# Performance work log

Measured on AMD Instinct MI355X. Metric: run time of the kernel, lower is better.

The kernel has to match this reference:

```python
import jax, jax.numpy as jnp
import numpy as np

N_NODES = 100000
N_EDGES = 1600000
NFEAT = 128
NHID = 128
NCLASS = 40
BN_EPS = 1e-5


def _glorot(key, shape):
    fan_in, fan_out = shape[1], shape[0]
    lim = (6.0 / (fan_in + fan_out)) ** 0.5
    return jax.random.uniform(key, shape, jnp.float32, -lim, lim)


def setup_inputs() -> dict:
    key = jax.random.key(0)
    ks = jax.random.split(key, 16)
    x = jax.random.normal(ks[0], (N_NODES, NFEAT), jnp.float32)
    src = jax.random.randint(ks[1], (N_EDGES,), 0, N_NODES, jnp.int64)
    dst = jax.random.randint(ks[2], (N_EDGES,), 0, N_NODES, jnp.int64)
    edge_index = jnp.stack([src, dst])  # [2, E]
    return {
        "x": x,
        "edge_index": edge_index,
        # conv1: nfeat -> nhid (lin_l with bias on aggregated msgs, lin_r no bias on root)
        "W1l": _glorot(ks[3], (NHID, NFEAT)), "b1": jnp.zeros((NHID,), jnp.float32),
        "W1r": _glorot(ks[4], (NHID, NFEAT)),
        # convx[0]: nhid -> nhid
        "Wxl": _glorot(ks[5], (NHID, NHID)), "bx": jnp.zeros((NHID,), jnp.float32),
        "Wxr": _glorot(ks[6], (NHID, NHID)),
        # conv2: nhid -> nclass
        "W2l": _glorot(ks[7], (NCLASS, NHID)), "b2": jnp.zeros((NCLASS,), jnp.float32),
        "W2r": _glorot(ks[8], (NCLASS, NHID)),
        # batch_norm3 (nhid) and batch_norm2 (nclass)
        "g3": jnp.ones((NHID,), jnp.float32), "be3": jnp.zeros((NHID,), jnp.float32),
        "g2": jnp.ones((NCLASS,), jnp.float32), "be2": jnp.zeros((NCLASS,), jnp.float32),
    }


def _sage_conv(x, src, dst, Wl, b, Wr):
    # mean aggregation of source features at destination nodes
    msg = x[src]                                                  # [E, F] gather
    agg = jax.ops.segment_sum(msg, dst, num_segments=N_NODES)    # [N, F] scatter-add
    cnt = jax.ops.segment_sum(jnp.ones((msg.shape[0],), x.dtype), dst, num_segments=N_NODES)
    mean = agg / jnp.maximum(cnt, 1.0)[:, None]                   # empty neighborhoods -> 0
    return mean @ Wl.T + b + x @ Wr.T


def _batch_norm(x, gamma, beta):
    mu = jnp.mean(x, axis=0)
    var = jnp.mean(jnp.square(x - mu), axis=0)  # biased var (training-mode BN)
    return (x - mu) * jax.lax.rsqrt(var + BN_EPS) * gamma + beta


def reference(x, edge_index, W1l, b1, W1r, Wxl, bx, Wxr, W2l, b2, W2r, g3, be3, g2, be2):
    src, dst = edge_index[0], edge_index[1]
    h = _sage_conv(x, src, dst, W1l, b1, W1r)      # conv1
    h = jax.nn.relu(h)
    # convx loop (nlayer - 2 == 1); dropout p=0 is identity
    h = _sage_conv(h, src, dst, Wxl, bx, Wxr)
    h = _batch_norm(h, g3, be3)                    # batch_norm3 (BN=True)
    h = jax.nn.relu(h)
    h = _sage_conv(h, src, dst, W2l, b2, W2r)      # conv2
    h = _batch_norm(h, g2, be2)                    # batch_norm2
    return h
```

## Files before the change

kernel.cpp:

```cpp
#include <hip/hip_runtime.h>
#include <hip/hip_bf16.h>

#define NN 100000
#define NE 1600000
#define NF 128
#define NC 40
#define BN_EPS 1e-5f

#define NB 256
#define NBU ((NN + 511) >> 9)
#define PT_TILE 4096
#define PT_GRID ((NE + PT_TILE - 1) / PT_TILE)
#define SBANK 32
#define NTILES (NN / 16)
#define LIN_GRID 1250
#define LIN80_GRID 512

typedef __attribute__((ext_vector_type(8))) short short8;
typedef __attribute__((ext_vector_type(4))) float float4v;
typedef __attribute__((ext_vector_type(4))) int int4v;

__device__ __forceinline__ unsigned short f2b(float f) {
    __hip_bfloat16 h = __float2bfloat16(f);
    return *reinterpret_cast<unsigned short*>(&h);
}
__device__ __forceinline__ float b2f_hi(unsigned u) { return __uint_as_float(u & 0xffff0000u); }
__device__ __forceinline__ float b2f_lo(unsigned u) { return __uint_as_float(u << 16); }


__global__ __launch_bounds__(256) void bhist_kernel(const int* __restrict__ dst,
                                                    int* __restrict__ bhist) {
    __shared__ int lh[NB];
    int tid = threadIdx.x;
    lh[tid] = 0;
    __syncthreads();
    int base = blockIdx.x * PT_TILE;
    int cnt = min(PT_TILE, NE - base);
    const int4v* d4 = (const int4v*)(dst + base);
    int cnt4 = cnt >> 2;
    for (int i = tid; i < cnt4; i += 256) {
        int4v d = __builtin_nontemporal_load(d4 + i);
        atomicAdd(&lh[d[0] >> 9], 1);
        atomicAdd(&lh[d[1] >> 9], 1);
        atomicAdd(&lh[d[2] >> 9], 1);
        atomicAdd(&lh[d[3] >> 9], 1);
    }
    __syncthreads();
    if (lh[tid]) atomicAdd(&bhist[tid], lh[tid]);
}

__global__ __launch_bounds__(256) void bscan_kernel(const int* __restrict__ bhist,
                                                    int* __restrict__ bbase,
                                                    int* __restrict__ bcur) {
    __shared__ int lds[NB];
    int t = threadIdx.x;
    int v = bhist[t];
    lds[t] = v;
    __syncthreads();
    for (int off = 1; off < NB; off <<= 1) {
        int u = (t >= off) ? lds[t - off] : 0;
        __syncthreads();
        lds[t] += u;
        __syncthreads();
    }
    int ex = lds[t] - v;
    bbase[t] = ex;
    bcur[t] = ex;
}

__global__ __launch_bounds__(256) void part_kernel(const int* __restrict__ src,
                                                   const int* __restrict__ dst,
                                                   int* __restrict__ bcur,
                                                   int2* __restrict__ stage) {
    __shared__ int2 pairs[PT_TILE];
    __shared__ int lhist[NB];
    __shared__ int gbase[NB];
    int tid = threadIdx.x;
    int base = blockIdx.x * PT_TILE;
    int cnt = min(PT_TILE, NE - base);
    int cnt4 = cnt >> 2;

    lhist[tid] = 0;
    __syncthreads();

    const int4v* d4 = (const int4v*)(dst + base);
    const int4v* s4 = (const int4v*)(src + base);
    for (int i = tid; i < cnt4; i += 256) {
        int4v d = __builtin_nontemporal_load(d4 + i);
        int4v s = __builtin_nontemporal_load(s4 + i);
#pragma unroll
        for (int j = 0; j < 4; ++j) {
            pairs[j * cnt4 + i] = make_int2(d[j], s[j]);
            atomicAdd(&lhist[d[j] >> 9], 1);
        }
    }
    __syncthreads();

    int c = lhist[tid];
    gbase[tid] = (c > 0) ? atomicAdd(&bcur[tid], c) : 0;
    lhist[tid] = 0;
    __syncthreads();

    for (int k = tid; k < cnt; k += 256) {
        int2 p = pairs[k];
        int b = p.x >> 9;
        int pos = atomicAdd(&lhist[b], 1);
        stage[gbase[b] + pos] = p;
    }
}


__global__ __launch_bounds__(512) void bucket_build_kernel(const long long* __restrict__ stage,
                                                           const int* __restrict__ bbase,
                                                           const int* __restrict__ bcur,
                                                           int* __restrict__ row_ptr,
                                                           float* __restrict__ inv_cnt,
                                                           int* __restrict__ csr) {
    __shared__ int hist[512];
    __shared__ int sa[512], sb[512];
    __shared__ int cur[512];
    int tid = threadIdx.x;
    int b = blockIdx.x;
    int s = bbase[b], e = bcur[b];

    hist[tid] = 0;
    __syncthreads();

    for (int i = s + tid; i < e; i += 512) {
        long long p = __builtin_nontemporal_load(stage + i);
        int dl = ((int)(p & 0xffffffffLL)) & 511;
        atomicAdd(&hist[dl], 1);
    }
    __syncthreads();

    sa[tid] = hist[tid];
    __syncthreads();
    int* pin = sa;
    int* pout = sb;
    for (int off = 1; off < 512; off <<= 1) {
        pout[tid] = pin[tid] + ((tid >= off) ? pin[tid - off] : 0);
        __syncthreads();
        int* t = pin; pin = pout; pout = t;
    }

    int d = hist[tid];
    int ex = pin[tid] - d;
    cur[tid] = ex;
    int n = b * 512 + tid;
    if (n < NN) {
        row_ptr[n] = s + ex;
        inv_cnt[n] = 1.0f / (float)(d > 0 ? d : 1);
    }
    if (b == 0 && tid == 0) row_ptr[NN] = NE;
    __syncthreads();

    for (int i = s + tid; i < e; i += 512) {
        long long p = __builtin_nontemporal_load(stage + i);
        int dl = ((int)(p & 0xffffffffLL)) & 511;
        int sv = (int)(p >> 32);
        int pos = atomicAdd(&cur[dl], 1);
        csr[s + pos] = sv;
    }
}


__global__ __launch_bounds__(256) void f2b4_kernel(const float* __restrict__ in,
                                                   unsigned short* __restrict__ out, int n4) {
    int i = blockIdx.x * 256 + threadIdx.x;
    if (i < n4) {
        float4 v = ((const float4*)in)[i];
        ushort4 o;
        o.x = f2b(v.x); o.y = f2b(v.y); o.z = f2b(v.z); o.w = f2b(v.w);
        ((ushort4*)out)[i] = o;
    }
}


__global__ __launch_bounds__(64) void pack_w_kernel(const float* __restrict__ Wl,
                                                    const float* __restrict__ Wr,
                                                    unsigned short* __restrict__ Bp) {
    int nt = blockIdx.x & 7;
    int kk = blockIdx.x >> 3;
    int lane = threadIdx.x;
    int n = nt * 16 + (lane & 15);
    int kb = kk * 32 + (lane >> 4) * 8;
    size_t base = ((size_t)(kk * 8 + nt) * 64 + lane) * 8;
#pragma unroll
    for (int j = 0; j < 8; ++j) {
        int k = kb + j;
        float v = (k < NF) ? Wl[(size_t)n * NF + k] : Wr[(size_t)n * NF + (k - NF)];
        Bp[base + j] = f2b(v);
    }
}

__global__ __launch_bounds__(64) void pack_w80_kernel(const float* __restrict__ Wl,
                                                      const float* __restrict__ Wr,
                                                      unsigned short* __restrict__ Bp) {
    int nt = blockIdx.x % 5;
    int kk = blockIdx.x / 5;
    int lane = threadIdx.x;
    int n = nt * 16 + (lane & 15);
    int kb = kk * 32 + (lane >> 4) * 8;
    size_t base = ((size_t)(kk * 5 + nt) * 64 + lane) * 8;
#pragma unroll
    for (int j = 0; j < 8; ++j) {
        int k = kb + j;
        float v = (n < NC) ? Wl[(size_t)n * NF + k] : Wr[(size_t)(n - NC) * NF + k];
        Bp[base + j] = f2b(v);
    }
}


__global__ __launch_bounds__(256) void agg_mean_bf16(const unsigned short* __restrict__ X,
                                                     const int* __restrict__ csr,
                                                     const int* __restrict__ row_ptr,
                                                     const float* __restrict__ inv_cnt,
                                                     unsigned short* __restrict__ out) {
    int tid = threadIdx.x;
    int lane = tid & 63;
    int wave = tid >> 6;
    int qw = lane >> 4;
    int sl = lane & 15;
    int n = blockIdx.x * 16 + wave * 4 + qw;
    if (n >= NN) return;
    int s = row_ptr[n], e = row_ptr[n + 1];
    int foff = sl * 8;

    float a[8];
#pragma unroll
    for (int j = 0; j < 8; ++j) a[j] = 0.f;

    int i = s;
    for (; i + 4 <= e; i += 4) {
        int s0 = csr[i], s1 = csr[i + 1], s2 = csr[i + 2], s3 = csr[i + 3];
        uint4 u0 = *(const uint4*)(X + (size_t)s0 * NF + foff);
        uint4 u1 = *(const uint4*)(X + (size_t)s1 * NF + foff);
        uint4 u2 = *(const uint4*)(X + (size_t)s2 * NF + foff);
        uint4 u3 = *(const uint4*)(X + (size_t)s3 * NF + foff);
        a[0] += b2f_lo(u0.x) + b2f_lo(u1.x) + b2f_lo(u2.x) + b2f_lo(u3.x);
        a[1] += b2f_hi(u0.x) + b2f_hi(u1.x) + b2f_hi(u2.x) + b2f_hi(u3.x);
        a[2] += b2f_lo(u0.y) + b2f_lo(u1.y) + b2f_lo(u2.y) + b2f_lo(u3.y);
        a[3] += b2f_hi(u0.y) + b2f_hi(u1.y) + b2f_hi(u2.y) + b2f_hi(u3.y);
        a[4] += b2f_lo(u0.z) + b2f_lo(u1.z) + b2f_lo(u2.z) + b2f_lo(u3.z);
        a[5] += b2f_hi(u0.z) + b2f_hi(u1.z) + b2f_hi(u2.z) + b2f_hi(u3.z);
        a[6] += b2f_lo(u0.w) + b2f_lo(u1.w) + b2f_lo(u2.w) + b2f_lo(u3.w);
        a[7] += b2f_hi(u0.w) + b2f_hi(u1.w) + b2f_hi(u2.w) + b2f_hi(u3.w);
    }
    for (; i < e; ++i) {
        uint4 u = *(const uint4*)(X + (size_t)csr[i] * NF + foff);
        a[0] += b2f_lo(u.x); a[1] += b2f_hi(u.x);
        a[2] += b2f_lo(u.y); a[3] += b2f_hi(u.y);
        a[4] += b2f_lo(u.z); a[5] += b2f_hi(u.z);
        a[6] += b2f_lo(u.w); a[7] += b2f_hi(u.w);
    }

    float ic = inv_cnt[n];
    uint4 o;
    o.x = (unsigned)f2b(a[0] * ic) | ((unsigned)f2b(a[1] * ic) << 16);
    o.y = (unsigned)f2b(a[2] * ic) | ((unsigned)f2b(a[3] * ic) << 16);
    o.z = (unsigned)f2b(a[4] * ic) | ((unsigned)f2b(a[5] * ic) << 16);
    o.w = (unsigned)f2b(a[6] * ic) | ((unsigned)f2b(a[7] * ic) << 16);
    *(uint4*)(out + (size_t)n * NF + foff) = o;
}


template <bool RELU, bool STATS>
__device__ __forceinline__ void lin_body(const unsigned short* __restrict__ Ab,
                                         const unsigned short* __restrict__ Xb,
                                         const unsigned short* __restrict__ Bp,
                                         const float* __restrict__ bias,
                                         unsigned short* __restrict__ outb,
                                         float* __restrict__ sums,
                                         float* ls) {
    int tid = threadIdx.x;
    int wave = tid >> 6;
    int lane = tid & 63;
    int quad = lane >> 4;
    int sl = lane & 15;
    const short8* Bv = (const short8*)Bp;

    if (STATS) {
        ls[tid] = 0.f;
        __syncthreads();
    }

    short8 bfr[8][2];
#pragma unroll
    for (int kk = 0; kk < 8; ++kk)
#pragma unroll
        for (int j = 0; j < 2; ++j)
            bfr[kk][j] = Bv[(kk * 8 + 2 * wave + j) * 64 + lane];

    float4 bias4[2];
#pragma unroll
    for (int j = 0; j < 2; ++j)
        bias4[j] = *(const float4*)(bias + (2 * wave + j) * 16 + quad * 4);

    float sts[2][4], stq[2][4];
    if (STATS) {
#pragma unroll
        for (int j = 0; j < 2; ++j)
#pragma unroll
            for (int r = 0; r < 4; ++r) { sts[j][r] = 0.f; stq[j][r] = 0.f; }
    }

    for (int t = blockIdx.x; t < NTILES; t += LIN_GRID) {
        int rr = t * 16 + sl;
        const unsigned short* arow = Ab + (size_t)rr * NF;
        const unsigned short* xrow = Xb + (size_t)rr * NF;

        short8 xf[8];
#pragma unroll
        for (int kk = 0; kk < 8; ++kk) {
            int kb = (kk & 3) * 32 + quad * 8;
            const unsigned short* asrc = (kk < 4) ? arow : xrow;
            xf[kk] = *(const short8*)(asrc + kb);
        }

        float4v acc[2];
#pragma unroll
        for (int j = 0; j < 2; ++j) acc[j] = (float4v){0.f, 0.f, 0.f, 0.f};

#pragma unroll
        for (int kk = 0; kk < 8; ++kk)
#pragma unroll
            for (int j = 0; j < 2; ++j)
                acc[j] = __builtin_amdgcn_mfma_f32_16x16x32_bf16(bfr[kk][j], xf[kk], acc[j], 0, 0, 0);

#pragma unroll
        for (int j = 0; j < 2; ++j) {
            int c0 = (2 * wave + j) * 16 + quad * 4;
            float v0 = acc[j][0] + bias4[j].x;
            float v1 = acc[j][1] + bias4[j].y;
            float v2 = acc[j][2] + bias4[j].z;
            float v3 = acc[j][3] + bias4[j].w;
            if (RELU) {
                v0 = fmaxf(v0, 0.f); v1 = fmaxf(v1, 0.f);
                v2 = fmaxf(v2, 0.f); v3 = fmaxf(v3, 0.f);
            }
            if (STATS) {
                sts[j][0] += v0; stq[j][0] += v0 * v0;
                sts[j][1] += v1; stq[j][1] += v1 * v1;
                sts[j][2] += v2; stq[j][2] += v2 * v2;
                sts[j][3] += v3; stq[j][3] += v3 * v3;
            }
            ushort4 o;
            o.x = f2b(v0); o.y = f2b(v1); o.z = f2b(v2); o.w = f2b(v3);
            *(ushort4*)(outb + (size_t)rr * NF + c0) = o;
        }
    }

    if (STATS) {
#pragma unroll
        for (int j = 0; j < 2; ++j) {
            int c0 = (2 * wave + j) * 16 + quad * 4;
#pragma unroll
            for (int r = 0; r < 4; ++r) {
                atomicAdd(&ls[c0 + r], sts[j][r]);
                atomicAdd(&ls[128 + c0 + r], stq[j][r]);
            }
        }
        __syncthreads();
        atomicAdd(&sums[(blockIdx.x & (SBANK - 1)) * 256 + tid], ls[tid]);
    }
}

__global__ __launch_bounds__(256, 3) void lin_conv1_kernel(const unsigned short* __restrict__ Ab,
                                                           const unsigned short* __restrict__ Xb,
                                                           const unsigned short* __restrict__ Bp,
                                                           const float* __restrict__ bias,
                                                           unsigned short* __restrict__ outb) {
    lin_body<true, false>(Ab, Xb, Bp, bias, outb, nullptr, nullptr);
}

__global__ __launch_bounds__(256, 3) void lin_convx_kernel(const unsigned short* __restrict__ Ab,
                                                           const unsigned short* __restrict__ Xb,
                                                           const unsigned short* __restrict__ Bp,
                                                           const float* __restrict__ bias,
                                                           unsigned short* __restrict__ outb,
                                                           float* __restrict__ sums) {
    __shared__ float ls[256];
    lin_body<false, true>(Ab, Xb, Bp, bias, outb, sums, ls);
}


__global__ __launch_bounds__(128) void bn3_coef_kernel(const float* __restrict__ sums,
                                                       const float* __restrict__ g,
                                                       const float* __restrict__ be,
                                                       float* __restrict__ sc,
                                                       float* __restrict__ sh) {
    int c = threadIdx.x;
    float sv = 0.f, qv = 0.f;
    for (int b = 0; b < SBANK; ++b) {
        sv += sums[b * 256 + c];
        qv += sums[b * 256 + 128 + c];
    }
    float invN = 1.0f / (float)NN;
    float mu = sv * invN;
    float var = qv * invN - mu * mu;
    float s = rsqrtf(var + BN_EPS) * g[c];
    sc[c] = s;
    sh[c] = be[c] - mu * s;
}


__global__ __launch_bounds__(256, 2) void lin80_mfma_kernel(const unsigned short* __restrict__ Xb,
                                                            const unsigned short* __restrict__ Bp,
                                                            const float* __restrict__ b2,
                                                            const float* __restrict__ bnsc,
                                                            const float* __restrict__ bnsh,
                                                            unsigned short* __restrict__ t40,
                                                            float* __restrict__ z40) {
    int tid = threadIdx.x;
    int wave = tid >> 6;
    int lane = tid & 63;
    int quad = lane >> 4;
    int sl = lane & 15;
    const short8* Bv = (const short8*)Bp;

    short8 bfr[4][5];
#pragma unroll
    for (int kk = 0; kk < 4; ++kk)
#pragma unroll
        for (int nt = 0; nt < 5; ++nt)
            bfr[kk][nt] = Bv[(kk * 5 + nt) * 64 + lane];

    float4 sc0[4], sc1[4], sh0[4], sh1[4];
#pragma unroll
    for (int kk = 0; kk < 4; ++kk) {
        int kb = kk * 32 + quad * 8;
        sc0[kk] = *(const float4*)(bnsc + kb);
        sc1[kk] = *(const float4*)(bnsc + kb + 4);
        sh0[kk] = *(const float4*)(bnsh + kb);
        sh1[kk] = *(const float4*)(bnsh + kb + 4);
    }

    int gw = blockIdx.x * 4 + wave;
    for (int t = gw; t < NTILES; t += LIN80_GRID * 4) {
        int rr = t * 16 + sl;
        const unsigned short* xrow = Xb + (size_t)rr * NF;

        float4v acc[5];
#pragma unroll
        for (int nt = 0; nt < 5; ++nt) acc[nt] = (float4v){0.f, 0.f, 0.f, 0.f};

#pragma unroll
        for (int kk = 0; kk < 4; ++kk) {
            uint4 u = *(const uint4*)(xrow + kk * 32 + quad * 8);
            short8 xf;
            xf[0] = (short)f2b(fmaxf(b2f_lo(u.x) * sc0[kk].x + sh0[kk].x, 0.f));
            xf[1] = (short)f2b(fmaxf(b2f_hi(u.x) * sc0[kk].y + sh0[kk].y, 0.f));
            xf[2] = (short)f2b(fmaxf(b2f_lo(u.y) * sc0[kk].z + sh0[kk].z, 0.f));
            xf[3] = (short)f2b(fmaxf(b2f_hi(u.y) * sc0[kk].w + sh0[kk].w, 0.f));
            xf[4] = (short)f2b(fmaxf(b2f_lo(u.z) * sc1[kk].x + sh1[kk].x, 0.f));
            xf[5] = (short)f2b(fmaxf(b2f_hi(u.z) * sc1[kk].y + sh1[kk].y, 0.f));
            xf[6] = (short)f2b(fmaxf(b2f_lo(u.w) * sc1[kk].z + sh1[kk].z, 0.f));
            xf[7] = (short)f2b(fmaxf(b2f_hi(u.w) * sc1[kk].w + sh1[kk].w, 0.f));
#pragma unroll
            for (int nt = 0; nt < 5; ++nt)
                acc[nt] = __builtin_amdgcn_mfma_f32_16x16x32_bf16(bfr[kk][nt], xf, acc[nt], 0, 0, 0);
        }

#pragma unroll
        for (int nt = 0; nt < 5; ++nt) {
            int c0 = nt * 16 + quad * 4;
            if (c0 < NC) {
                ushort4 o;
                o.x = f2b(acc[nt][0]); o.y = f2b(acc[nt][1]);
                o.z = f2b(acc[nt][2]); o.w = f2b(acc[nt][3]);
                *(ushort4*)(t40 + (size_t)rr * NC + c0) = o;
            } else {
                float4 bz = *(const float4*)(b2 + c0 - NC);
                float4 o;
                o.x = acc[nt][0] + bz.x; o.y = acc[nt][1] + bz.y;
                o.z = acc[nt][2] + bz.z; o.w = acc[nt][3] + bz.w;
                *(float4*)(z40 + (size_t)rr * NC + (c0 - NC)) = o;
            }
        }
    }
}


__global__ __launch_bounds__(256) void agg40_add_bf16(const unsigned short* __restrict__ T,
                                                      const float* __restrict__ Z,
                                                      const int* __restrict__ csr,
                                                      const int* __restrict__ row_ptr,
                                                      const float* __restrict__ inv_cnt,
                                                      float* __restrict__ out) {
    int tid = threadIdx.x;
    int lane = tid & 63;
    int wave = tid >> 6;
    if (lane >= 60) return;
    int sub = lane / 20;
    int sl = lane % 20;
    int n = blockIdx.x * 12 + wave * 3 + sub;
    if (n >= NN) return;
    int s = row_ptr[n], e = row_ptr[n + 1];
    const unsigned short* Tf = T + sl * 2;
    float a0 = 0.f, a1 = 0.f;
    int i = s;
    for (; i + 4 <= e; i += 4) {
        int s0 = csr[i], s1 = csr[i + 1], s2 = csr[i + 2], s3 = csr[i + 3];
        unsigned u0 = *(const unsigned*)(Tf + (size_t)s0 * NC);
        unsigned u1 = *(const unsigned*)(Tf + (size_t)s1 * NC);
        unsigned u2 = *(const unsigned*)(Tf + (size_t)s2 * NC);
        unsigned u3 = *(const unsigned*)(Tf + (size_t)s3 * NC);
        a0 += b2f_lo(u0) + b2f_lo(u1) + b2f_lo(u2) + b2f_lo(u3);
        a1 += b2f_hi(u0) + b2f_hi(u1) + b2f_hi(u2) + b2f_hi(u3);
    }
    for (; i < e; ++i) {
        unsigned u = *(const unsigned*)(Tf + (size_t)csr[i] * NC);
        a0 += b2f_lo(u);
        a1 += b2f_hi(u);
    }
    float ic = inv_cnt[n];
    const float2 zv = *(const float2*)(Z + (size_t)n * NC + sl * 2);
    float2 o;
    o.x = a0 * ic + zv.x;
    o.y = a1 * ic + zv.y;
    *(float2*)(out + (size_t)n * NC + sl * 2) = o;
}

#define BN_GRID 640

template <int F>
__global__ __launch_bounds__(256) void bn_stats2_kernel(const float* __restrict__ X,
                                                        float* __restrict__ sums) {
    __shared__ float ls[2 * F];
    int tid = threadIdx.x;
    for (int i = tid; i < 2 * F; i += 256) ls[i] = 0.f;
    __syncthreads();

    const int total4 = NN * F / 4;
    const int stride = BN_GRID * 256;
    int i0 = blockIdx.x * 256 + tid;
    int c0 = (i0 * 4) % F;
    float s0 = 0.f, s1 = 0.f, s2 = 0.f, s3 = 0.f;
    float q0 = 0.f, q1 = 0.f, q2 = 0.f, q3 = 0.f;
    for (int i = i0; i < total4; i += stride) {
        float4 v = ((const float4*)X)[i];
        s0 += v.x; q0 += v.x * v.x;
        s1 += v.y; q1 += v.y * v.y;
        s2 += v.z; q2 += v.z * v.z;
        s3 += v.w; q3 += v.w * v.w;
    }
    atomicAdd(&ls[c0 + 0], s0); atomicAdd(&ls[F + c0 + 0], q0);
    atomicAdd(&ls[c0 + 1], s1); atomicAdd(&ls[F + c0 + 1], q1);
    atomicAdd(&ls[c0 + 2], s2); atomicAdd(&ls[F + c0 + 2], q2);
    atomicAdd(&ls[c0 + 3], s3); atomicAdd(&ls[F + c0 + 3], q3);
    __syncthreads();
    for (int i = tid; i < 2 * F; i += 256) atomicAdd(&sums[i], ls[i]);
}

template <bool RELU>
__global__ __launch_bounds__(256) void bn_apply_kernel(float* __restrict__ X,
                                                       const float* __restrict__ sums,
                                                       const float* __restrict__ g,
                                                       const float* __restrict__ be,
                                                       int F, float invN) {
    size_t idx = (size_t)blockIdx.x * blockDim.x + threadIdx.x;
    size_t total = (size_t)NN * F;
    if (idx >= total) return;
    int t = (int)(idx % F);
    float mu = sums[t] * invN;
    float var = sums[F + t] * invN - mu * mu;
    float scale = rsqrtf(var + BN_EPS) * g[t];
    float v = (X[idx] - mu) * scale + be[t];
    if (RELU) v = fmaxf(v, 0.f);
    X[idx] = v;
}


extern "C" void kernel_launch(void* const* d_in, const int* in_sizes, int n_in,
                              void* d_out, int out_size, void* d_ws, size_t ws_size,
                              hipStream_t stream) {
    const float* x   = (const float*)d_in[0];
    const int*   ei  = (const int*)d_in[1];
    const int*   srcv = ei;
    const int*   dstv = ei + NE;
    const float* W1l = (const float*)d_in[2];
    const float* b1  = (const float*)d_in[3];
    const float* W1r = (const float*)d_in[4];
    const float* Wxl = (const float*)d_in[5];
    const float* bx  = (const float*)d_in[6];
    const float* Wxr = (const float*)d_in[7];
    const float* W2l = (const float*)d_in[8];
    const float* b2  = (const float*)d_in[9];
    const float* W2r = (const float*)d_in[10];
    const float* g3  = (const float*)d_in[11];
    const float* be3 = (const float*)d_in[12];
    const float* g2  = (const float*)d_in[13];
    const float* be2 = (const float*)d_in[14];
    float* out = (float*)d_out;

    char* w = (char*)d_ws;
    unsigned short* xb   = (unsigned short*)w; w += (size_t)NN * NF * 2;
    unsigned short* h1b  = (unsigned short*)w; w += (size_t)NN * NF * 2;
    unsigned short* aggb = (unsigned short*)w; w += (size_t)NN * NF * 2;
    unsigned short* h2b  = (unsigned short*)w; w += (size_t)NN * NF * 2;
    int* csr     = (int*)w; w += (size_t)NE * 4;
    int* row_ptr = (int*)w; w += (size_t)(NN + 4) * 4;
    float* inv_cnt = (float*)w; w += (size_t)NN * 4;
    float* bnbuf3  = (float*)w; w += (size_t)SBANK * 256 * 4;
    float* bnbuf2  = (float*)w; w += 2 * NC * 4;
    float* bnsc    = (float*)w; w += NF * 4;
    float* bnsh    = (float*)w; w += NF * 4;
    unsigned short* Bp1 = (unsigned short*)w; w += (size_t)256 * NF * 2;
    unsigned short* Bpx = (unsigned short*)w; w += (size_t)256 * NF * 2;
    unsigned short* Bp2 = (unsigned short*)w; w += (size_t)128 * 80 * 2;
    int* bhist = (int*)w; w += NB * 4;
    int* bbase = (int*)w; w += NB * 4;
    int* bcurA = (int*)w; w += NB * 4;
    int2* stage = (int2*)h2b;
    unsigned short* t40 = xb;
    float* z40 = (float*)h1b;

    hipMemsetAsync(bhist, 0, NB * 4, stream);
    hipMemsetAsync(bnbuf3, 0, (size_t)SBANK * 256 * 4, stream);
    hipMemsetAsync(bnbuf2, 0, 2 * NC * 4, stream);

    bhist_kernel<<<PT_GRID, 256, 0, stream>>>(dstv, bhist);
    bscan_kernel<<<1, 256, 0, stream>>>(bhist, bbase, bcurA);
    part_kernel<<<PT_GRID, 256, 0, stream>>>(srcv, dstv, bcurA, stage);
    bucket_build_kernel<<<NBU, 512, 0, stream>>>((const long long*)stage, bbase, bcurA,
                                                 row_ptr, inv_cnt, csr);

    f2b4_kernel<<<(NN * NF / 4 + 255) / 256, 256, 0, stream>>>(x, xb, NN * NF / 4);
    pack_w_kernel<<<64, 64, 0, stream>>>(W1l, W1r, Bp1);
    pack_w_kernel<<<64, 64, 0, stream>>>(Wxl, Wxr, Bpx);
    pack_w80_kernel<<<20, 64, 0, stream>>>(W2l, W2r, Bp2);

    const int nblk_agg = (NN + 15) / 16;

    agg_mean_bf16<<<nblk_agg, 256, 0, stream>>>(xb, csr, row_ptr, inv_cnt, aggb);
    lin_conv1_kernel<<<LIN_GRID, 256, 0, stream>>>(aggb, xb, Bp1, b1, h1b);

    agg_mean_bf16<<<nblk_agg, 256, 0, stream>>>(h1b, csr, row_ptr, inv_cnt, aggb);
    lin_convx_kernel<<<LIN_GRID, 256, 0, stream>>>(aggb, h1b, Bpx, bx, h2b, bnbuf3);

    bn3_coef_kernel<<<1, 128, 0, stream>>>(bnbuf3, g3, be3, bnsc, bnsh);

    lin80_mfma_kernel<<<LIN80_GRID, 256, 0, stream>>>(h2b, Bp2, b2, bnsc, bnsh, t40, z40);
    agg40_add_bf16<<<(NN + 11) / 12, 256, 0, stream>>>(t40, z40, csr, row_ptr, inv_cnt, out);

    bn_stats2_kernel<NC><<<BN_GRID, 256, 0, stream>>>(out, bnbuf2);
    bn_apply_kernel<false><<<(NN * NC + 255) / 256, 256, 0, stream>>>(out, bnbuf2, g2, be2, NC, 1.0f / NN);
}
```

Before: 481.9 us.

## Fuse BN2 stats into agg40, restructure linear kernels with LDS weights and prefetch

The final batch-norm statistics are now accumulated inside the agg40 aggregation kernel through shared-memory atomics and 64 global banks. This removes a separate full pass over the output, and a small coefficient kernel then feeds a simpler per-element apply. The 128-wide linear kernels now use 512-thread blocks in which each wave handles one 16-column slice. Weights are staged in LDS, and each block processes a fixed run of 10 tiles with double-buffered row loads and scheduling barriers. The trade-offs are more LDS atomics in the aggregation kernel and higher LDS use per block in the linear kernels.

```diff
diff --git a/kernel.cpp b/kernel.cpp
--- a/kernel.cpp
+++ b/kernel.cpp
@@ -12,8 +12,10 @@
 #define PT_TILE 4096
 #define PT_GRID ((NE + PT_TILE - 1) / PT_TILE)
 #define SBANK 32
+#define NBANK2 64
 #define NTILES (NN / 16)
-#define LIN_GRID 1250
+#define LIN_BLKS 625
+#define TILES_PER_BLK 10
 #define LIN80_GRID 512
 
 typedef __attribute__((ext_vector_type(8))) short short8;
@@ -271,116 +273,107 @@
                                          const float* __restrict__ bias,
                                          unsigned short* __restrict__ outb,
                                          float* __restrict__ sums,
-                                         float* ls) {
+                                         short8* Bs, float* ls) {
     int tid = threadIdx.x;
-    int wave = tid >> 6;
+    int w = tid >> 6;
     int lane = tid & 63;
     int quad = lane >> 4;
     int sl = lane & 15;
+
     const short8* Bv = (const short8*)Bp;
-
-    if (STATS) {
-        ls[tid] = 0.f;
-        __syncthreads();
-    }
-
-    short8 bfr[8][2];
-#pragma unroll
-    for (int kk = 0; kk < 8; ++kk)
-#pragma unroll
-        for (int j = 0; j < 2; ++j)
-            bfr[kk][j] = Bv[(kk * 8 + 2 * wave + j) * 64 + lane];
-
-    float4 bias4[2];
-#pragma unroll
-    for (int j = 0; j < 2; ++j)
-        bias4[j] = *(const float4*)(bias + (2 * wave + j) * 16 + quad * 4);
-
-    float sts[2][4], stq[2][4];
-    if (STATS) {
-#pragma unroll
-        for (int j = 0; j < 2; ++j)
-#pragma unroll
-            for (int r = 0; r < 4; ++r) { sts[j][r] = 0.f; stq[j][r] = 0.f; }
-    }
-
-    for (int t = blockIdx.x; t < NTILES; t += LIN_GRID) {
+    for (int i = tid; i < 4096; i += 512) Bs[i] = Bv[i];
+    if (STATS && tid < 256) ls[tid] = 0.f;
+    __syncthreads();
+
+    float4 bias4 = *(const float4*)(bias + w * 16 + quad * 4);
+
+    float sv[4], qv[4];
+#pragma unroll
+    for (int r = 0; r < 4; ++r) { sv[r] = 0.f; qv[r] = 0.f; }
+
+    int tbase = blockIdx.x * TILES_PER_BLK;
+    short8 xa[8], xb_[8];
+
+    auto issue = [&](short8* buf, int t) {
         int rr = t * 16 + sl;
         const unsigned short* arow = Ab + (size_t)rr * NF;
         const unsigned short* xrow = Xb + (size_t)rr * NF;
-
-        short8 xf[8];
 #pragma unroll
         for (int kk = 0; kk < 8; ++kk) {
             int kb = (kk & 3) * 32 + quad * 8;
-            const unsigned short* asrc = (kk < 4) ? arow : xrow;
-            xf[kk] = *(const short8*)(asrc + kb);
-        }
-
-        float4v acc[2];
-#pragma unroll
-        for (int j = 0; j < 2; ++j) acc[j] = (float4v){0.f, 0.f, 0.f, 0.f};
-
-#pragma unroll
-        for (int kk = 0; kk < 8; ++kk)
-#pragma unroll
-            for (int j = 0; j < 2; ++j)
-                acc[j] = __builtin_amdgcn_mfma_f32_16x16x32_bf16(bfr[kk][j], xf[kk], acc[j], 0, 0, 0);
-
-#pragma unroll
-        for (int j = 0; j < 2; ++j) {
-            int c0 = (2 * wave + j) * 16 + quad * 4;
-            float v0 = acc[j][0] + bias4[j].x;
-            float v1 = acc[j][1] + bias4[j].y;
-            float v2 = acc[j][2] + bias4[j].z;
-            float v3 = acc[j][3] + bias4[j].w;
-            if (RELU) {
-                v0 = fmaxf(v0, 0.f); v1 = fmaxf(v1, 0.f);
-                v2 = fmaxf(v2, 0.f); v3 = fmaxf(v3, 0.f);
-            }
-            if (STATS) {
-                sts[j][0] += v0; stq[j][0] += v0 * v0;
-                sts[j][1] += v1; stq[j][1] += v1 * v1;
-                sts[j][2] += v2; stq[j][2] += v2 * v2;
-                sts[j][3] += v3; stq[j][3] += v3 * v3;
-            }
-            ushort4 o;
-            o.x = f2b(v0); o.y = f2b(v1); o.z = f2b(v2); o.w = f2b(v3);
-            *(ushort4*)(outb + (size_t)rr * NF + c0) = o;
-        }
+            buf[kk] = *(const short8*)(((kk < 4) ? arow : xrow) + kb);
+        }
+    };
+
+    auto compute = [&](short8* buf, int t) {
+        float4v acc = (float4v){0.f, 0.f, 0.f, 0.f};
+#pragma unroll
+        for (int kk = 0; kk < 8; ++kk) {
+            short8 bfr = Bs[(kk * 8 + w) * 64 + lane];
+            acc = __builtin_amdgcn_mfma_f32_16x16x32_bf16(bfr, buf[kk], acc, 0, 0, 0);
+        }
+        int rr = t * 16 + sl;
+        int c0 = w * 16 + quad * 4;
+        float v0 = acc[0] + bias4.x;
+        float v1 = acc[1] + bias4.y;
+        float v2 = acc[2] + bias4.z;
+        float v3 = acc[3] + bias4.w;
+        if (RELU) {
+            v0 = fmaxf(v0, 0.f); v1 = fmaxf(v1, 0.f);
+            v2 = fmaxf(v2, 0.f); v3 = fmaxf(v3, 0.f);
+        }
+        if (STATS) {
+            sv[0] += v0; qv[0] += v0 * v0;
+            sv[1] += v1; qv[1] += v1 * v1;
+            sv[2] += v2; qv[2] += v2 * v2;
+            sv[3] += v3; qv[3] += v3 * v3;
+        }
+        ushort4 o;
+        o.x = f2b(v0); o.y = f2b(v1); o.z = f2b(v2); o.w = f2b(v3);
+        *(ushort4*)(outb + (size_t)rr * NF + c0) = o;
+    };
+
+    issue(xa, tbase);
+#pragma unroll
+    for (int i = 0; i < TILES_PER_BLK; i += 2) {
+        issue(xb_, tbase + i + 1);
+        __builtin_amdgcn_sched_barrier(0);
+        compute(xa, tbase + i);
+        if (i + 2 < TILES_PER_BLK) issue(xa, tbase + i + 2);
+        __builtin_amdgcn_sched_barrier(0);
+        compute(xb_, tbase + i + 1);
     }
 
     if (STATS) {
-#pragma unroll
-        for (int j = 0; j < 2; ++j) {
-            int c0 = (2 * wave + j) * 16 + quad * 4;
-#pragma unroll
-            for (int r = 0; r < 4; ++r) {
-                atomicAdd(&ls[c0 + r], sts[j][r]);
-                atomicAdd(&ls[128 + c0 + r], stq[j][r]);
-            }
+        int c0 = w * 16 + quad * 4;
+#pragma unroll
+        for (int r = 0; r < 4; ++r) {
+            atomicAdd(&ls[c0 + r], sv[r]);
+            atomicAdd(&ls[128 + c0 + r], qv[r]);
         }
         __syncthreads();
-        atomicAdd(&sums[(blockIdx.x & (SBANK - 1)) * 256 + tid], ls[tid]);
-    }
-}
-
-__global__ __launch_bounds__(256, 3) void lin_conv1_kernel(const unsigned short* __restrict__ Ab,
+        if (tid < 256) atomicAdd(&sums[(blockIdx.x & (SBANK - 1)) * 256 + tid], ls[tid]);
+    }
+}
+
+__global__ __launch_bounds__(512, 4) void lin_conv1_kernel(const unsigned short* __restrict__ Ab,
                                                            const unsigned short* __restrict__ Xb,
                                                            const unsigned short* __restrict__ Bp,
                                                            const float* __restrict__ bias,
                                                            unsigned short* __restrict__ outb) {
-    lin_body<true, false>(Ab, Xb, Bp, bias, outb, nullptr, nullptr);
-}
-
-__global__ __launch_bounds__(256, 3) void lin_convx_kernel(const unsigned short* __restrict__ Ab,
+    __shared__ short8 Bs[4096];
+    lin_body<true, false>(Ab, Xb, Bp, bias, outb, nullptr, Bs, nullptr);
+}
+
+__global__ __launch_bounds__(512, 4) void lin_convx_kernel(const unsigned short* __restrict__ Ab,
                                                            const unsigned short* __restrict__ Xb,
                                                            const unsigned short* __restrict__ Bp,
                                                            const float* __restrict__ bias,
                                                            unsigned short* __restrict__ outb,
                                                            float* __restrict__ sums) {
+    __shared__ short8 Bs[4096];
     __shared__ float ls[256];
-    lin_body<false, true>(Ab, Xb, Bp, bias, outb, sums, ls);
+    lin_body<false, true>(Ab, Xb, Bp, bias, outb, sums, Bs, ls);
 }
 
 
@@ -486,88 +479,82 @@
                                                       const int* __restrict__ csr,
                                                       const int* __restrict__ row_ptr,
                                                       const float* __restrict__ inv_cnt,
-                                                      float* __restrict__ out) {
+                                                      float* __restrict__ out,
+                                                      float* __restrict__ sums2) {
+    __shared__ float ls[80];
     int tid = threadIdx.x;
+    if (tid < 80) ls[tid] = 0.f;
+    __syncthreads();
+
     int lane = tid & 63;
     int wave = tid >> 6;
-    if (lane >= 60) return;
     int sub = lane / 20;
     int sl = lane % 20;
     int n = blockIdx.x * 12 + wave * 3 + sub;
-    if (n >= NN) return;
-    int s = row_ptr[n], e = row_ptr[n + 1];
-    const unsigned short* Tf = T + sl * 2;
-    float a0 = 0.f, a1 = 0.f;
-    int i = s;
-    for (; i + 4 <= e; i += 4) {
-        int s0 = csr[i], s1 = csr[i + 1], s2 = csr[i + 2], s3 = csr[i + 3];
-        unsigned u0 = *(const unsigned*)(Tf + (size_t)s0 * NC);
-        unsigned u1 = *(const unsigned*)(Tf + (size_t)s1 * NC);
-        unsigned u2 = *(const unsigned*)(Tf + (size_t)s2 * NC);
-        unsigned u3 = *(const unsigned*)(Tf + (size_t)s3 * NC);
-        a0 += b2f_lo(u0) + b2f_lo(u1) + b2f_lo(u2) + b2f_lo(u3);
-        a1 += b2f_hi(u0) + b2f_hi(u1) + b2f_hi(u2) + b2f_hi(u3);
-    }
-    for (; i < e; ++i) {
-        unsigned u = *(const unsigned*)(Tf + (size_t)csr[i] * NC);
-        a0 += b2f_lo(u);
-        a1 += b2f_hi(u);
-    }
-    float ic = inv_cnt[n];
-    const float2 zv = *(const float2*)(Z + (size_t)n * NC + sl * 2);
-    float2 o;
-    o.x = a0 * ic + zv.x;
-    o.y = a1 * ic + zv.y;
-    *(float2*)(out + (size_t)n * NC + sl * 2) = o;
-}
-
-#define BN_GRID 640
-
-template <int F>
-__global__ __launch_bounds__(256) void bn_stats2_kernel(const float* __restrict__ X,
-                                                        float* __restrict__ sums) {
-    __shared__ float ls[2 * F];
-    int tid = threadIdx.x;
-    for (int i = tid; i < 2 * F; i += 256) ls[i] = 0.f;
-    __syncthreads();
-
-    const int total4 = NN * F / 4;
-    const int stride = BN_GRID * 256;
-    int i0 = blockIdx.x * 256 + tid;
-    int c0 = (i0 * 4) % F;
-    float s0 = 0.f, s1 = 0.f, s2 = 0.f, s3 = 0.f;
-    float q0 = 0.f, q1 = 0.f, q2 = 0.f, q3 = 0.f;
-    for (int i = i0; i < total4; i += stride) {
-        float4 v = ((const float4*)X)[i];
-        s0 += v.x; q0 += v.x * v.x;
-        s1 += v.y; q1 += v.y * v.y;
-        s2 += v.z; q2 += v.z * v.z;
-        s3 += v.w; q3 += v.w * v.w;
-    }
-    atomicAdd(&ls[c0 + 0], s0); atomicAdd(&ls[F + c0 + 0], q0);
-    atomicAdd(&ls[c0 + 1], s1); atomicAdd(&ls[F + c0 + 1], q1);
-    atomicAdd(&ls[c0 + 2], s2); atomicAdd(&ls[F + c0 + 2], q2);
-    atomicAdd(&ls[c0 + 3], s3); atomicAdd(&ls[F + c0 + 3], q3);
-    __syncthreads();
-    for (int i = tid; i < 2 * F; i += 256) atomicAdd(&sums[i], ls[i]);
-}
-
-template <bool RELU>
-__global__ __launch_bounds__(256) void bn_apply_kernel(float* __restrict__ X,
-                                                       const float* __restrict__ sums,
-                                                       const float* __restrict__ g,
-                                                       const float* __restrict__ be,
-                                                       int F, float invN) {
+    bool act = (lane < 60) && (n < NN);
+
+    if (act) {
+        int s = row_ptr[n], e = row_ptr[n + 1];
+        const unsigned short* Tf = T + sl * 2;
+        float a0 = 0.f, a1 = 0.f;
+        int i = s;
+        for (; i + 4 <= e; i += 4) {
+            int s0 = csr[i], s1 = csr[i + 1], s2 = csr[i + 2], s3 = csr[i + 3];
+            unsigned u0 = *(const unsigned*)(Tf + (size_t)s0 * NC);
+            unsigned u1 = *(const unsigned*)(Tf + (size_t)s1 * NC);
+            unsigned u2 = *(const unsigned*)(Tf + (size_t)s2 * NC);
+            unsigned u3 = *(const unsigned*)(Tf + (size_t)s3 * NC);
+            a0 += b2f_lo(u0) + b2f_lo(u1) + b2f_lo(u2) + b2f_lo(u3);
+            a1 += b2f_hi(u0) + b2f_hi(u1) + b2f_hi(u2) + b2f_hi(u3);
+        }
+        for (; i < e; ++i) {
+            unsigned u = *(const unsigned*)(Tf + (size_t)csr[i] * NC);
+            a0 += b2f_lo(u);
+            a1 += b2f_hi(u);
+        }
+        float ic = inv_cnt[n];
+        const float2 zv = *(const float2*)(Z + (size_t)n * NC + sl * 2);
+        float ox = a0 * ic + zv.x;
+        float oy = a1 * ic + zv.y;
+        float2 o; o.x = ox; o.y = oy;
+        *(float2*)(out + (size_t)n * NC + sl * 2) = o;
+        atomicAdd(&ls[2 * sl + 0], ox);
+        atomicAdd(&ls[2 * sl + 1], oy);
+        atomicAdd(&ls[NC + 2 * sl + 0], ox * ox);
+        atomicAdd(&ls[NC + 2 * sl + 1], oy * oy);
+    }
+    __syncthreads();
+    if (tid < 80) atomicAdd(&sums2[(blockIdx.x & (NBANK2 - 1)) * 80 + tid], ls[tid]);
+}
+
+
+__global__ __launch_bounds__(64) void bn2_coef_kernel(const float* __restrict__ sums2,
+                                                      const float* __restrict__ g,
+                                                      const float* __restrict__ be,
+                                                      float* __restrict__ sc,
+                                                      float* __restrict__ sh) {
+    int c = threadIdx.x;
+    if (c >= NC) return;
+    float s = 0.f, q = 0.f;
+    for (int b = 0; b < NBANK2; ++b) {
+        s += sums2[b * 80 + c];
+        q += sums2[b * 80 + NC + c];
+    }
+    float invN = 1.0f / (float)NN;
+    float mu = s * invN;
+    float var = q * invN - mu * mu;
+    float scv = rsqrtf(var + BN_EPS) * g[c];
+    sc[c] = scv;
+    sh[c] = be[c] - mu * scv;
+}
+
+__global__ __launch_bounds__(256) void bn2_apply_kernel(float* __restrict__ X,
+                                                        const float* __restrict__ sc,
+                                                        const float* __restrict__ sh) {
     size_t idx = (size_t)blockIdx.x * blockDim.x + threadIdx.x;
-    size_t total = (size_t)NN * F;
-    if (idx >= total) return;
-    int t = (int)(idx % F);
-    float mu = sums[t] * invN;
-    float var = sums[F + t] * invN - mu * mu;
-    float scale = rsqrtf(var + BN_EPS) * g[t];
-    float v = (X[idx] - mu) * scale + be[t];
-    if (RELU) v = fmaxf(v, 0.f);
-    X[idx] = v;
+    if (idx >= (size_t)NN * NC) return;
+    int c = (int)(idx % NC);
+    X[idx] = X[idx] * sc[c] + sh[c];
 }
 
 
@@ -602,9 +589,11 @@
     int* row_ptr = (int*)w; w += (size_t)(NN + 4) * 4;
     float* inv_cnt = (float*)w; w += (size_t)NN * 4;
     float* bnbuf3  = (float*)w; w += (size_t)SBANK * 256 * 4;
-    float* bnbuf2  = (float*)w; w += 2 * NC * 4;
+    float* sums2   = (float*)w; w += (size_t)NBANK2 * 80 * 4;
     float* bnsc    = (float*)w; w += NF * 4;
     float* bnsh    = (float*)w; w += NF * 4;
+    float* sc2     = (float*)w; w += 64 * 4;
+    float* sh2     = (float*)w; w += 64 * 4;
     unsigned short* Bp1 = (unsigned short*)w; w += (size_t)256 * NF * 2;
     unsigned short* Bpx = (unsigned short*)w; w += (size_t)256 * NF * 2;
     unsigned short* Bp2 = (unsigned short*)w; w += (size_t)128 * 80 * 2;
@@ -617,7 +606,7 @@
 
     hipMemsetAsync(bhist, 0, NB * 4, stream);
     hipMemsetAsync(bnbuf3, 0, (size_t)SBANK * 256 * 4, stream);
-    hipMemsetAsync(bnbuf2, 0, 2 * NC * 4, stream);
+    hipMemsetAsync(sums2, 0, (size_t)NBANK2 * 80 * 4, stream);
 
     bhist_kernel<<<PT_GRID, 256, 0, stream>>>(dstv, bhist);
     bscan_kernel<<<1, 256, 0, stream>>>(bhist, bbase, bcurA);
@@ -633,16 +622,16 @@
     const int nblk_agg = (NN + 15) / 16;
 
     agg_mean_bf16<<<nblk_agg, 256, 0, stream>>>(xb, csr, row_ptr, inv_cnt, aggb);
-    lin_conv1_kernel<<<LIN_GRID, 256, 0, stream>>>(aggb, xb, Bp1, b1, h1b);
+    lin_conv1_kernel<<<LIN_BLKS, 512, 0, stream>>>(aggb, xb, Bp1, b1, h1b);
 
     agg_mean_bf16<<<nblk_agg, 256, 0, stream>>>(h1b, csr, row_ptr, inv_cnt, aggb);
-    lin_convx_kernel<<<LIN_GRID, 256, 0, stream>>>(aggb, h1b, Bpx, bx, h2b, bnbuf3);
+    lin_convx_kernel<<<LIN_BLKS, 512, 0, stream>>>(aggb, h1b, Bpx, bx, h2b, bnbuf3);
 
     bn3_coef_kernel<<<1, 128, 0, stream>>>(bnbuf3, g3, be3, bnsc, bnsh);
 
     lin80_mfma_kernel<<<LIN80_GRID, 256, 0, stream>>>(h2b, Bp2, b2, bnsc, bnsh, t40, z40);
-    agg40_add_bf16<<<(NN + 11) / 12, 256, 0, stream>>>(t40, z40, csr, row_ptr, inv_cnt, out);
-
-    bn_stats2_kernel<NC><<<BN_GRID, 256, 0, stream>>>(out, bnbuf2);
-    bn_apply_kernel<false><<<(NN * NC + 255) / 256, 256, 0, stream>>>(out, bnbuf2, g2, be2, NC, 1.0f / NN);
-}
+    agg40_add_bf16<<<(NN + 11) / 12, 256, 0, stream>>>(t40, z40, csr, row_ptr, inv_cnt, out, sums2);
+
+    bn2_coef_kernel<<<1, 64, 0, stream>>>(sums2, g2, be2, sc2, sh2);
+    bn2_apply_kernel<<<(NN * NC + 255) / 256, 256, 0, stream>>>(out, sc2, sh2);
+}
```

Result: slower. 531.6 us (+10.3%).

## Split SAGE linear kernels by output half and double-buffer input tiles in LDS

Applied to the files above, without the earlier changes.

The two 128-wide SAGE linear kernels now launch twice as many blocks, each computing one half of the output columns. Weights are staged in shared memory, and the A/X row tiles are loaded coalesced into a swizzled, double-buffered LDS tile so the next tile's global load overlaps the current MFMA work. The BN stats bank count is doubled, and each half writes only its own channels. This trades register-resident weights for LDS reads plus per-tile barriers, and it re-reads the input rows once per column half.

```diff
diff --git a/kernel.cpp b/kernel.cpp
--- a/kernel.cpp
+++ b/kernel.cpp
@@ -11,9 +11,10 @@
 #define NBU ((NN + 511) >> 9)
 #define PT_TILE 4096
 #define PT_GRID ((NE + PT_TILE - 1) / PT_TILE)
-#define SBANK 32
+#define SBANK 64
 #define NTILES (NN / 16)
 #define LIN_GRID 1250
+#define LIN_TILES 5
 #define LIN80_GRID 512
 
 typedef __attribute__((ext_vector_type(8))) short short8;
@@ -271,97 +272,102 @@
                                          const float* __restrict__ bias,
                                          unsigned short* __restrict__ outb,
                                          float* __restrict__ sums,
-                                         float* ls) {
+                                         uint4* Bsv, uint4* Tls, float* ls) {
     int tid = threadIdx.x;
     int wave = tid >> 6;
     int lane = tid & 63;
     int quad = lane >> 4;
     int sl = lane & 15;
-    const short8* Bv = (const short8*)Bp;
+    int h = blockIdx.x & 1;
+    int b0 = blockIdx.x >> 1;
+    int nt = h * 4 + wave;
+
+    const uint4* Bg = (const uint4*)Bp;
+#pragma unroll
+    for (int j = 0; j < 8; ++j) {
+        int s = j * 256 + tid;
+        int l = s >> 6, ln = s & 63;
+        int gf = (l >> 2) * 8 + h * 4 + (l & 3);
+        Bsv[s] = Bg[gf * 64 + ln];
+    }
+    if (STATS) ls[tid] = 0.f;
+
+    int row0 = tid >> 4, cs = tid & 15;
+    int wslot = row0 * 16 + (cs ^ (row0 & 7));
+    {
+        int rr = b0 * 16 + row0;
+        uint4 ra = *(const uint4*)(Ab + (size_t)rr * NF + cs * 8);
+        uint4 rx = *(const uint4*)(Xb + (size_t)rr * NF + cs * 8);
+        Tls[wslot] = ra;
+        Tls[256 + wslot] = rx;
+    }
+    __syncthreads();
+
+    float4 bias4 = *(const float4*)(bias + nt * 16 + quad * 4);
+    float sv[4], qv[4];
+#pragma unroll
+    for (int r = 0; r < 4; ++r) { sv[r] = 0.f; qv[r] = 0.f; }
+
+#pragma unroll
+    for (int i = 0; i < LIN_TILES; ++i) {
+        const int cur = i & 1;
+        const int nxt = cur ^ 1;
+        int t = b0 + i * LIN_GRID;
+
+        uint4 ra, rx;
+        if (i + 1 < LIN_TILES) {
+            int rr1 = (b0 + (i + 1) * LIN_GRID) * 16 + row0;
+            ra = *(const uint4*)(Ab + (size_t)rr1 * NF + cs * 8);
+            rx = *(const uint4*)(Xb + (size_t)rr1 * NF + cs * 8);
+        }
+
+        float4v acc = (float4v){0.f, 0.f, 0.f, 0.f};
+#pragma unroll
+        for (int kk = 0; kk < 8; ++kk) {
+            int kcol = (kk & 3) * 4 + quad;
+            int xslot = cur * 512 + ((kk < 4) ? 0 : 256) + sl * 16 + (kcol ^ (sl & 7));
+            short8 xf = *(const short8*)(Tls + xslot);
+            short8 bf = *(const short8*)(Bsv + (kk * 4 + wave) * 64 + lane);
+            acc = __builtin_amdgcn_mfma_f32_16x16x32_bf16(bf, xf, acc, 0, 0, 0);
+        }
+
+        int rr = t * 16 + sl;
+        int c0 = nt * 16 + quad * 4;
+        float v0 = acc[0] + bias4.x;
+        float v1 = acc[1] + bias4.y;
+        float v2 = acc[2] + bias4.z;
+        float v3 = acc[3] + bias4.w;
+        if (RELU) {
+            v0 = fmaxf(v0, 0.f); v1 = fmaxf(v1, 0.f);
+            v2 = fmaxf(v2, 0.f); v3 = fmaxf(v3, 0.f);
+        }
+        if (STATS) {
+            sv[0] += v0; qv[0] += v0 * v0;
+            sv[1] += v1; qv[1] += v1 * v1;
+            sv[2] += v2; qv[2] += v2 * v2;
+            sv[3] += v3; qv[3] += v3 * v3;
+        }
+        ushort4 o;
+        o.x = f2b(v0); o.y = f2b(v1); o.z = f2b(v2); o.w = f2b(v3);
+        *(ushort4*)(outb + (size_t)rr * NF + c0) = o;
+
+        if (i + 1 < LIN_TILES) {
+            Tls[nxt * 512 + wslot] = ra;
+            Tls[nxt * 512 + 256 + wslot] = rx;
+        }
+        __syncthreads();
+    }
 
     if (STATS) {
-        ls[tid] = 0.f;
+        int c0 = nt * 16 + quad * 4;
+#pragma unroll
+        for (int r = 0; r < 4; ++r) {
+            atomicAdd(&ls[c0 + r], sv[r]);
+            atomicAdd(&ls[128 + c0 + r], qv[r]);
+        }
         __syncthreads();
-    }
-
-    short8 bfr[8][2];
-#pragma unroll
-    for (int kk = 0; kk < 8; ++kk)
-#pragma unroll
-        for (int j = 0; j < 2; ++j)
-            bfr[kk][j] = Bv[(kk * 8 + 2 * wave + j) * 64 + lane];
-
-    float4 bias4[2];
-#pragma unroll
-    for (int j = 0; j < 2; ++j)
-        bias4[j] = *(const float4*)(bias + (2 * wave + j) * 16 + quad * 4);
-
-    float sts[2][4], stq[2][4];
-    if (STATS) {
-#pragma unroll
-        for (int j = 0; j < 2; ++j)
-#pragma unroll
-            for (int r = 0; r < 4; ++r) { sts[j][r] = 0.f; stq[j][r] = 0.f; }
-    }
-
-    for (int t = blockIdx.x; t < NTILES; t += LIN_GRID) {
-        int rr = t * 16 + sl;
-        const unsigned short* arow = Ab + (size_t)rr * NF;
-        const unsigned short* xrow = Xb + (size_t)rr * NF;
-
-        short8 xf[8];
-#pragma unroll
-        for (int kk = 0; kk < 8; ++kk) {
-            int kb = (kk & 3) * 32 + quad * 8;
-            const unsigned short* asrc = (kk < 4) ? arow : xrow;
-            xf[kk] = *(const short8*)(asrc + kb);
-        }
-
-        float4v acc[2];
-#pragma unroll
-        for (int j = 0; j < 2; ++j) acc[j] = (float4v){0.f, 0.f, 0.f, 0.f};
-
-#pragma unroll
-        for (int kk = 0; kk < 8; ++kk)
-#pragma unroll
-            for (int j = 0; j < 2; ++j)
-                acc[j] = __builtin_amdgcn_mfma_f32_16x16x32_bf16(bfr[kk][j], xf[kk], acc[j], 0, 0, 0);
-
-#pragma unroll
-        for (int j = 0; j < 2; ++j) {
-            int c0 = (2 * wave + j) * 16 + quad * 4;
-            float v0 = acc[j][0] + bias4[j].x;
-            float v1 = acc[j][1] + bias4[j].y;
-            float v2 = acc[j][2] + bias4[j].z;
-            float v3 = acc[j][3] + bias4[j].w;
-            if (RELU) {
-                v0 = fmaxf(v0, 0.f); v1 = fmaxf(v1, 0.f);
-                v2 = fmaxf(v2, 0.f); v3 = fmaxf(v3, 0.f);
-            }
-            if (STATS) {
-                sts[j][0] += v0; stq[j][0] += v0 * v0;
-                sts[j][1] += v1; stq[j][1] += v1 * v1;
-                sts[j][2] += v2; stq[j][2] += v2 * v2;
-                sts[j][3] += v3; stq[j][3] += v3 * v3;
-            }
-            ushort4 o;
-            o.x = f2b(v0); o.y = f2b(v1); o.z = f2b(v2); o.w = f2b(v3);
-            *(ushort4*)(outb + (size_t)rr * NF + c0) = o;
-        }
-    }
-
-    if (STATS) {
-#pragma unroll
-        for (int j = 0; j < 2; ++j) {
-            int c0 = (2 * wave + j) * 16 + quad * 4;
-#pragma unroll
-            for (int r = 0; r < 4; ++r) {
-                atomicAdd(&ls[c0 + r], sts[j][r]);
-                atomicAdd(&ls[128 + c0 + r], stq[j][r]);
-            }
-        }
-        __syncthreads();
-        atomicAdd(&sums[(blockIdx.x & (SBANK - 1)) * 256 + tid], ls[tid]);
+        if (((tid & 127) >> 6) == h)
+            atomicAdd(&sums[(blockIdx.x & (SBANK - 1)) * 256 + tid], ls[tid]);
     }
 }
 
@@ -370,7 +376,9 @@
                                                            const unsigned short* __restrict__ Bp,
                                                            const float* __restrict__ bias,
                                                            unsigned short* __restrict__ outb) {
-    lin_body<true, false>(Ab, Xb, Bp, bias, outb, nullptr, nullptr);
+    __shared__ uint4 Bsv[2048];
+    __shared__ uint4 Tls[1024];
+    lin_body<true, false>(Ab, Xb, Bp, bias, outb, nullptr, Bsv, Tls, nullptr);
 }
 
 __global__ __launch_bounds__(256, 3) void lin_convx_kernel(const unsigned short* __restrict__ Ab,
@@ -379,8 +387,10 @@
                                                            const float* __restrict__ bias,
                                                            unsigned short* __restrict__ outb,
                                                            float* __restrict__ sums) {
+    __shared__ uint4 Bsv[2048];
+    __shared__ uint4 Tls[1024];
     __shared__ float ls[256];
-    lin_body<false, true>(Ab, Xb, Bp, bias, outb, sums, ls);
+    lin_body<false, true>(Ab, Xb, Bp, bias, outb, sums, Bsv, Tls, ls);
 }
 
 
@@ -633,10 +643,10 @@
     const int nblk_agg = (NN + 15) / 16;
 
     agg_mean_bf16<<<nblk_agg, 256, 0, stream>>>(xb, csr, row_ptr, inv_cnt, aggb);
-    lin_conv1_kernel<<<LIN_GRID, 256, 0, stream>>>(aggb, xb, Bp1, b1, h1b);
+    lin_conv1_kernel<<<2 * LIN_GRID, 256, 0, stream>>>(aggb, xb, Bp1, b1, h1b);
 
     agg_mean_bf16<<<nblk_agg, 256, 0, stream>>>(h1b, csr, row_ptr, inv_cnt, aggb);
-    lin_convx_kernel<<<LIN_GRID, 256, 0, stream>>>(aggb, h1b, Bpx, bx, h2b, bnbuf3);
+    lin_convx_kernel<<<2 * LIN_GRID, 256, 0, stream>>>(aggb, h1b, Bpx, bx, h2b, bnbuf3);
 
     bn3_coef_kernel<<<1, 128, 0, stream>>>(bnbuf3, g3, be3, bnsc, bnsh);
 
```

Result: faster. 468.6 us (-2.8%).
